# Kernel tuning notes

Hardware: AMD Instinct MI355X
Metric: run time of the kernel (lower is better)

The kernel has to match this reference:

```python
import jax, jax.numpy as jnp
import numpy as np

T, D, H, O = 16384, 512, 1024, 512


def setup_inputs() -> dict:
    key = jax.random.key(0)
    k_in, k_h0, kU, kW, kV = jax.random.split(key, 5)
    inputs = jax.random.randint(k_in, (T,), 0, D)
    h0 = jax.random.normal(k_h0, (H,), dtype=jnp.float32)
    U = jax.random.normal(kU, (H, D), dtype=jnp.float32) * 0.01
    W = jax.random.normal(kW, (H, H), dtype=jnp.float32) * 0.01
    V = jax.random.normal(kV, (O, H), dtype=jnp.float32) * 0.01
    bh = jnp.zeros((H,), dtype=jnp.float32)
    by = jnp.zeros((O,), dtype=jnp.float32)
    return {"inputs": inputs, "h0": h0, "U": U, "W": W, "V": V, "bh": bh, "by": by}


def reference(inputs, h0, U, W, V, bh, by):
    # U @ one_hot(x_t) is just a column gather of U; precompute for all t: (T, H)
    Ux = U.T[inputs]

    def step(h, ux):
        h = jnp.tanh(ux + W @ h + bh)  # (H,)
        return h, h

    h_T, hs = jax.lax.scan(step, h0, Ux)  # hs: (T, H)
    logits = hs @ V.T + by  # (T, O)
    return logits, h_T
```

## Files before the change

kernel.cpp:

```cpp
#include <hip/hip_runtime.h>
#include <cstdint>


constexpr int T_STEPS = 16384;
constexpr int D_DIM   = 512;
constexpr int H_DIM   = 1024;
constexpr int O_DIM   = 512;
constexpr int NBLK    = 32;
constexpr int NTHR    = 512;

__device__ __forceinline__ float fast_tanh(float x) {
    float e = __expf(2.f * x);
    return 1.f - 2.f / (e + 1.f);
}

__device__ __forceinline__ float hsum4(const float4& v) {
    return (v.x + v.y) + (v.z + v.w);
}

__global__ __launch_bounds__(NTHR, 2)
void rnn_fused(const int* __restrict__ xs, const float* __restrict__ h0,
               const float* __restrict__ U, const float* __restrict__ W,
               const float* __restrict__ V, const float* __restrict__ bh,
               const float* __restrict__ by, float* __restrict__ out,
               unsigned long long* __restrict__ htag)
{
    const int b   = blockIdx.x;
    const int tid = threadIdx.x;
    const int w   = tid >> 6;
    const int l   = tid & 63;

    __shared__ float hl[2][H_DIM];

    const int wr0 = b * 32 + w * 4;
    float4 wreg[4][4];
#pragma unroll
    for (int j = 0; j < 4; ++j)
#pragma unroll
        for (int q = 0; q < 4; ++q)
            wreg[j][q] = *(const float4*)(W + (size_t)(wr0 + j) * H_DIM + 16 * l + 4 * q);
    const float bh_r = bh[wr0 + (l & 3)];
    const int   urow = wr0 + (l & 3);

    const int vr0 = b * 16 + w * 2;
    float4 vreg[2][4];
#pragma unroll
    for (int m = 0; m < 2; ++m)
#pragma unroll
        for (int q = 0; q < 4; ++q)
            vreg[m][q] = *(const float4*)(V + (size_t)(vr0 + m) * H_DIM + 16 * l + 4 * q);
    const float by_r = by[vr0 + (l & 1)];

    int rdw[4];
#pragma unroll
    for (int q = 0; q < 4; ++q)
        rdw[q] = 16 * l + 4 * (q ^ ((l >> 1) & 3));
    const int c   = tid >> 3;
    const int qw  = (tid >> 1) & 3;
    const int wdw = 16 * c + 4 * (qw ^ ((c >> 1) & 3)) + 2 * (tid & 1);

    const bool o1 = (l & 1) != 0, o2 = (l & 2) != 0;

    for (int t = 0; t < T_STEPS; ++t) {
        const int sb = (~t) & 1;
        float* hb = hl[sb];

        const int   xt = xs[t];
        const float uv = U[(size_t)urow * D_DIM + xt];

        float2 hpair;
        if (t == 0) {
            hpair = *(const float2*)(h0 + 2 * tid);
        } else {
            const unsigned want = (unsigned)(t - 1);
            const unsigned long long* pp = htag + (size_t)((t - 1) & 1) * H_DIM + 2 * tid;
            unsigned long long q0, q1;
            do {
                q0 = __hip_atomic_load(pp + 0, __ATOMIC_RELAXED, __HIP_MEMORY_SCOPE_AGENT);
                q1 = __hip_atomic_load(pp + 1, __ATOMIC_RELAXED, __HIP_MEMORY_SCOPE_AGENT);
            } while ((unsigned)(q0 >> 32) != want || (unsigned)(q1 >> 32) != want);
            hpair = make_float2(__uint_as_float((unsigned)q0),
                                __uint_as_float((unsigned)q1));
        }
        *(float2*)&hb[wdw] = hpair;
        __syncthreads();

        float4 h4[4];
#pragma unroll
        for (int q = 0; q < 4; ++q) h4[q] = *(const float4*)&hb[rdw[q]];

        float s[4];
#pragma unroll
        for (int j = 0; j < 4; ++j) {
            float4 a = make_float4(0.f, 0.f, 0.f, 0.f);
#pragma unroll
            for (int q = 0; q < 4; ++q) {
                a.x += wreg[j][q].x * h4[q].x;
                a.y += wreg[j][q].y * h4[q].y;
                a.z += wreg[j][q].z * h4[q].z;
                a.w += wreg[j][q].w * h4[q].w;
            }
            s[j] = hsum4(a);
        }
        float A  = o1 ? s[1] : s[0], Ax = o1 ? s[0] : s[1];
        float B  = o1 ? s[3] : s[2], Bx = o1 ? s[2] : s[3];
        A += __shfl_xor(Ax, 1);
        B += __shfl_xor(Bx, 1);
        float Cv = o2 ? B : A, Cx = o2 ? A : B;
        Cv += __shfl_xor(Cx, 2);
        Cv += __shfl_xor(Cv, 4);
        Cv += __shfl_xor(Cv, 8);
        Cv += __shfl_xor(Cv, 16);
        Cv += __shfl_xor(Cv, 32);

        const float hv = fast_tanh(Cv + bh_r + uv);
        if (l < 4) {
            const unsigned long long pk =
                ((unsigned long long)(unsigned)t << 32) | (unsigned long long)__float_as_uint(hv);
            __hip_atomic_store(htag + (size_t)(t & 1) * H_DIM + wr0 + l, pk,
                               __ATOMIC_RELAXED, __HIP_MEMORY_SCOPE_AGENT);
        }

        if (t > 0) {
            float sv[2];
#pragma unroll
            for (int m = 0; m < 2; ++m) {
                float4 a = make_float4(0.f, 0.f, 0.f, 0.f);
#pragma unroll
                for (int q = 0; q < 4; ++q) {
                    a.x += vreg[m][q].x * h4[q].x;
                    a.y += vreg[m][q].y * h4[q].y;
                    a.z += vreg[m][q].z * h4[q].z;
                    a.w += vreg[m][q].w * h4[q].w;
                }
                sv[m] = hsum4(a);
            }
            float P  = o1 ? sv[1] : sv[0], Px = o1 ? sv[0] : sv[1];
            P += __shfl_xor(Px, 1);
            P += __shfl_xor(P, 2);
            P += __shfl_xor(P, 4);
            P += __shfl_xor(P, 8);
            P += __shfl_xor(P, 16);
            P += __shfl_xor(P, 32);
            if (l < 2) out[(size_t)(t - 1) * O_DIM + vr0 + l] = P + by_r;
        }
    }

    {
        const unsigned want = (unsigned)(T_STEPS - 1);
        const unsigned long long* pp = htag + (size_t)((T_STEPS - 1) & 1) * H_DIM + 2 * tid;
        unsigned long long q0, q1;
        do {
            q0 = __hip_atomic_load(pp + 0, __ATOMIC_RELAXED, __HIP_MEMORY_SCOPE_AGENT);
            q1 = __hip_atomic_load(pp + 1, __ATOMIC_RELAXED, __HIP_MEMORY_SCOPE_AGENT);
        } while ((unsigned)(q0 >> 32) != want || (unsigned)(q1 >> 32) != want);
        float2 hpair = make_float2(__uint_as_float((unsigned)q0),
                                   __uint_as_float((unsigned)q1));
        if (b == 0)
            *(float2*)&out[(size_t)T_STEPS * O_DIM + 2 * tid] = hpair;

        float* hb = hl[1];
        *(float2*)&hb[wdw] = hpair;
        __syncthreads();
        float4 h4[4];
#pragma unroll
        for (int q = 0; q < 4; ++q) h4[q] = *(const float4*)&hb[rdw[q]];
        float sv[2];
#pragma unroll
        for (int m = 0; m < 2; ++m) {
            float4 a = make_float4(0.f, 0.f, 0.f, 0.f);
#pragma unroll
            for (int q = 0; q < 4; ++q) {
                a.x += vreg[m][q].x * h4[q].x;
                a.y += vreg[m][q].y * h4[q].y;
                a.z += vreg[m][q].z * h4[q].z;
                a.w += vreg[m][q].w * h4[q].w;
            }
            sv[m] = hsum4(a);
        }
        float P  = o1 ? sv[1] : sv[0], Px = o1 ? sv[0] : sv[1];
        P += __shfl_xor(Px, 1);
        P += __shfl_xor(P, 2);
        P += __shfl_xor(P, 4);
        P += __shfl_xor(P, 8);
        P += __shfl_xor(P, 16);
        P += __shfl_xor(P, 32);
        if (l < 2) out[(size_t)(T_STEPS - 1) * O_DIM + vr0 + l] = P + by_r;
    }
}

extern "C" void kernel_launch(void* const* d_in, const int* in_sizes, int n_in,
                              void* d_out, int out_size, void* d_ws, size_t ws_size,
                              hipStream_t stream) {
    const int*   xs = (const int*)d_in[0];
    const float* h0 = (const float*)d_in[1];
    const float* U  = (const float*)d_in[2];
    const float* W  = (const float*)d_in[3];
    const float* V  = (const float*)d_in[4];
    const float* bh = (const float*)d_in[5];
    const float* by = (const float*)d_in[6];
    float* out = (float*)d_out;

    unsigned long long* htag = (unsigned long long*)d_ws;
    hipMemsetAsync(d_ws, 0xAA, 2 * H_DIM * sizeof(unsigned long long), stream);

    rnn_fused<<<NBLK, NTHR, 0, stream>>>(xs, h0, U, W, V, bh, by, out, htag);
}
```

Measured before the change: 23.19 ms.

## Have each wave poll the full hidden vector directly, dropping LDS staging and barrier

Each wavefront now loads the entire tagged hidden state from global memory with inline-asm system-coherent dwordx4 loads, checked wave-wide with __all. This replaces the per-thread partial poll followed by an LDS exchange and __syncthreads. It removes the block-wide barrier and the LDS round trip from the serial critical path of every timestep. In exchange each wave issues 8x more polling traffic against the shared workspace, and the weight layout is reorganized into float2 slices.

```diff
diff --git a/kernel.cpp b/kernel.cpp
--- a/kernel.cpp
+++ b/kernel.cpp
@@ -9,16 +9,18 @@
 constexpr int NBLK    = 32;
 constexpr int NTHR    = 512;
 
+typedef unsigned int u32x4 __attribute__((ext_vector_type(4)));
+
 __device__ __forceinline__ float fast_tanh(float x) {
     float e = __expf(2.f * x);
     return 1.f - 2.f / (e + 1.f);
 }
 
-__device__ __forceinline__ float hsum4(const float4& v) {
-    return (v.x + v.y) + (v.z + v.w);
-}
-
-__global__ __launch_bounds__(NTHR, 2)
+#define POLL_ISSUE(reg, addr)                                          \
+    asm volatile("global_load_dwordx4 %0, %1, off sc0 sc1"             \
+                 : "=v"(reg) : "v"((unsigned long long)(addr)))
+
+__global__ __launch_bounds__(NTHR, 1)
 void rnn_fused(const int* __restrict__ xs, const float* __restrict__ h0,
                const float* __restrict__ U, const float* __restrict__ W,
                const float* __restrict__ V, const float* __restrict__ bh,
@@ -30,80 +32,74 @@
     const int w   = tid >> 6;
     const int l   = tid & 63;
 
-    __shared__ float hl[2][H_DIM];
-
     const int wr0 = b * 32 + w * 4;
-    float4 wreg[4][4];
+    float2 wreg[4][8];
 #pragma unroll
     for (int j = 0; j < 4; ++j)
 #pragma unroll
-        for (int q = 0; q < 4; ++q)
-            wreg[j][q] = *(const float4*)(W + (size_t)(wr0 + j) * H_DIM + 16 * l + 4 * q);
+        for (int i = 0; i < 8; ++i)
+            wreg[j][i] = *(const float2*)(W + (size_t)(wr0 + j) * H_DIM + 128 * i + 2 * l);
     const float bh_r = bh[wr0 + (l & 3)];
     const int   urow = wr0 + (l & 3);
 
     const int vr0 = b * 16 + w * 2;
-    float4 vreg[2][4];
+    float2 vreg[2][8];
 #pragma unroll
     for (int m = 0; m < 2; ++m)
 #pragma unroll
-        for (int q = 0; q < 4; ++q)
-            vreg[m][q] = *(const float4*)(V + (size_t)(vr0 + m) * H_DIM + 16 * l + 4 * q);
+        for (int i = 0; i < 8; ++i)
+            vreg[m][i] = *(const float2*)(V + (size_t)(vr0 + m) * H_DIM + 128 * i + 2 * l);
     const float by_r = by[vr0 + (l & 1)];
 
-    int rdw[4];
-#pragma unroll
-    for (int q = 0; q < 4; ++q)
-        rdw[q] = 16 * l + 4 * (q ^ ((l >> 1) & 3));
-    const int c   = tid >> 3;
-    const int qw  = (tid >> 1) & 3;
-    const int wdw = 16 * c + 4 * (qw ^ ((c >> 1) & 3)) + 2 * (tid & 1);
+    const unsigned long long* gp0 = htag + 2 * l;
+    const unsigned long long* gp1 = htag + H_DIM + 2 * l;
 
     const bool o1 = (l & 1) != 0, o2 = (l & 2) != 0;
 
+    float2 h2[8];
+
     for (int t = 0; t < T_STEPS; ++t) {
-        const int sb = (~t) & 1;
-        float* hb = hl[sb];
-
         const int   xt = xs[t];
         const float uv = U[(size_t)urow * D_DIM + xt];
 
-        float2 hpair;
         if (t == 0) {
-            hpair = *(const float2*)(h0 + 2 * tid);
+#pragma unroll
+            for (int i = 0; i < 8; ++i)
+                h2[i] = *(const float2*)(h0 + 128 * i + 2 * l);
         } else {
+            const unsigned long long* pp = ((t - 1) & 1) ? gp1 : gp0;
             const unsigned want = (unsigned)(t - 1);
-            const unsigned long long* pp = htag + (size_t)((t - 1) & 1) * H_DIM + 2 * tid;
-            unsigned long long q0, q1;
-            do {
-                q0 = __hip_atomic_load(pp + 0, __ATOMIC_RELAXED, __HIP_MEMORY_SCOPE_AGENT);
-                q1 = __hip_atomic_load(pp + 1, __ATOMIC_RELAXED, __HIP_MEMORY_SCOPE_AGENT);
-            } while ((unsigned)(q0 >> 32) != want || (unsigned)(q1 >> 32) != want);
-            hpair = make_float2(__uint_as_float((unsigned)q0),
-                                __uint_as_float((unsigned)q1));
-        }
-        *(float2*)&hb[wdw] = hpair;
-        __syncthreads();
-
-        float4 h4[4];
-#pragma unroll
-        for (int q = 0; q < 4; ++q) h4[q] = *(const float4*)&hb[rdw[q]];
-
-        float s[4];
-#pragma unroll
-        for (int j = 0; j < 4; ++j) {
-            float4 a = make_float4(0.f, 0.f, 0.f, 0.f);
-#pragma unroll
-            for (int q = 0; q < 4; ++q) {
-                a.x += wreg[j][q].x * h4[q].x;
-                a.y += wreg[j][q].y * h4[q].y;
-                a.z += wreg[j][q].z * h4[q].z;
-                a.w += wreg[j][q].w * h4[q].w;
+            u32x4 q[8];
+            for (;;) {
+#pragma unroll
+                for (int i = 0; i < 8; ++i) POLL_ISSUE(q[i], pp + 128 * i);
+                asm volatile("s_waitcnt vmcnt(0)" ::: "memory");
+                __builtin_amdgcn_sched_barrier(0);
+                bool ok = true;
+#pragma unroll
+                for (int i = 0; i < 8; ++i)
+                    ok = ok && (q[i].y == want) && (q[i].w == want);
+                if (__all(ok)) break;
             }
-            s[j] = hsum4(a);
-        }
-        float A  = o1 ? s[1] : s[0], Ax = o1 ? s[0] : s[1];
-        float B  = o1 ? s[3] : s[2], Bx = o1 ? s[2] : s[3];
+#pragma unroll
+            for (int i = 0; i < 8; ++i)
+                h2[i] = make_float2(__uint_as_float(q[i].x),
+                                    __uint_as_float(q[i].z));
+        }
+
+        float2 a0 = {0.f, 0.f}, a1 = {0.f, 0.f}, a2 = {0.f, 0.f}, a3 = {0.f, 0.f};
+#pragma unroll
+        for (int i = 0; i < 8; ++i) {
+            a0.x += wreg[0][i].x * h2[i].x; a0.y += wreg[0][i].y * h2[i].y;
+            a1.x += wreg[1][i].x * h2[i].x; a1.y += wreg[1][i].y * h2[i].y;
+            a2.x += wreg[2][i].x * h2[i].x; a2.y += wreg[2][i].y * h2[i].y;
+            a3.x += wreg[3][i].x * h2[i].x; a3.y += wreg[3][i].y * h2[i].y;
+        }
+        const float s0 = a0.x + a0.y, s1 = a1.x + a1.y;
+        const float s2 = a2.x + a2.y, s3 = a3.x + a3.y;
+
+        float A  = o1 ? s1 : s0, Ax = o1 ? s0 : s1;
+        float B  = o1 ? s3 : s2, Bx = o1 ? s2 : s3;
         A += __shfl_xor(Ax, 1);
         B += __shfl_xor(Bx, 1);
         float Cv = o2 ? B : A, Cx = o2 ? A : B;
@@ -116,26 +112,22 @@
         const float hv = fast_tanh(Cv + bh_r + uv);
         if (l < 4) {
             const unsigned long long pk =
-                ((unsigned long long)(unsigned)t << 32) | (unsigned long long)__float_as_uint(hv);
+                ((unsigned long long)(unsigned)t << 32) |
+                (unsigned long long)__float_as_uint(hv);
             __hip_atomic_store(htag + (size_t)(t & 1) * H_DIM + wr0 + l, pk,
                                __ATOMIC_RELAXED, __HIP_MEMORY_SCOPE_AGENT);
         }
+        __builtin_amdgcn_sched_barrier(0);
 
         if (t > 0) {
-            float sv[2];
-#pragma unroll
-            for (int m = 0; m < 2; ++m) {
-                float4 a = make_float4(0.f, 0.f, 0.f, 0.f);
-#pragma unroll
-                for (int q = 0; q < 4; ++q) {
-                    a.x += vreg[m][q].x * h4[q].x;
-                    a.y += vreg[m][q].y * h4[q].y;
-                    a.z += vreg[m][q].z * h4[q].z;
-                    a.w += vreg[m][q].w * h4[q].w;
-                }
-                sv[m] = hsum4(a);
+            float2 p0 = {0.f, 0.f}, p1 = {0.f, 0.f};
+#pragma unroll
+            for (int i = 0; i < 8; ++i) {
+                p0.x += vreg[0][i].x * h2[i].x; p0.y += vreg[0][i].y * h2[i].y;
+                p1.x += vreg[1][i].x * h2[i].x; p1.y += vreg[1][i].y * h2[i].y;
             }
-            float P  = o1 ? sv[1] : sv[0], Px = o1 ? sv[0] : sv[1];
+            const float sv0 = p0.x + p0.y, sv1 = p1.x + p1.y;
+            float P  = o1 ? sv1 : sv0, Px = o1 ? sv0 : sv1;
             P += __shfl_xor(Px, 1);
             P += __shfl_xor(P, 2);
             P += __shfl_xor(P, 4);
@@ -147,38 +139,39 @@
     }
 
     {
+        const unsigned long long* pp = gp1;
         const unsigned want = (unsigned)(T_STEPS - 1);
-        const unsigned long long* pp = htag + (size_t)((T_STEPS - 1) & 1) * H_DIM + 2 * tid;
-        unsigned long long q0, q1;
-        do {
-            q0 = __hip_atomic_load(pp + 0, __ATOMIC_RELAXED, __HIP_MEMORY_SCOPE_AGENT);
-            q1 = __hip_atomic_load(pp + 1, __ATOMIC_RELAXED, __HIP_MEMORY_SCOPE_AGENT);
-        } while ((unsigned)(q0 >> 32) != want || (unsigned)(q1 >> 32) != want);
-        float2 hpair = make_float2(__uint_as_float((unsigned)q0),
-                                   __uint_as_float((unsigned)q1));
-        if (b == 0)
-            *(float2*)&out[(size_t)T_STEPS * O_DIM + 2 * tid] = hpair;
-
-        float* hb = hl[1];
-        *(float2*)&hb[wdw] = hpair;
-        __syncthreads();
-        float4 h4[4];
-#pragma unroll
-        for (int q = 0; q < 4; ++q) h4[q] = *(const float4*)&hb[rdw[q]];
-        float sv[2];
-#pragma unroll
-        for (int m = 0; m < 2; ++m) {
-            float4 a = make_float4(0.f, 0.f, 0.f, 0.f);
-#pragma unroll
-            for (int q = 0; q < 4; ++q) {
-                a.x += vreg[m][q].x * h4[q].x;
-                a.y += vreg[m][q].y * h4[q].y;
-                a.z += vreg[m][q].z * h4[q].z;
-                a.w += vreg[m][q].w * h4[q].w;
-            }
-            sv[m] = hsum4(a);
-        }
-        float P  = o1 ? sv[1] : sv[0], Px = o1 ? sv[0] : sv[1];
+        u32x4 q[8];
+        for (;;) {
+#pragma unroll
+            for (int i = 0; i < 8; ++i) POLL_ISSUE(q[i], pp + 128 * i);
+            asm volatile("s_waitcnt vmcnt(0)" ::: "memory");
+            __builtin_amdgcn_sched_barrier(0);
+            bool ok = true;
+#pragma unroll
+            for (int i = 0; i < 8; ++i)
+                ok = ok && (q[i].y == want) && (q[i].w == want);
+            if (__all(ok)) break;
+        }
+#pragma unroll
+        for (int i = 0; i < 8; ++i)
+            h2[i] = make_float2(__uint_as_float(q[i].x),
+                                __uint_as_float(q[i].z));
+
+        if (b == 0 && w == 0) {
+#pragma unroll
+            for (int i = 0; i < 8; ++i)
+                *(float2*)&out[(size_t)T_STEPS * O_DIM + 128 * i + 2 * l] = h2[i];
+        }
+
+        float2 p0 = {0.f, 0.f}, p1 = {0.f, 0.f};
+#pragma unroll
+        for (int i = 0; i < 8; ++i) {
+            p0.x += vreg[0][i].x * h2[i].x; p0.y += vreg[0][i].y * h2[i].y;
+            p1.x += vreg[1][i].x * h2[i].x; p1.y += vreg[1][i].y * h2[i].y;
+        }
+        const float sv0 = p0.x + p0.y, sv1 = p1.x + p1.y;
+        float P  = o1 ? sv1 : sv0, Px = o1 ? sv0 : sv1;
         P += __shfl_xor(Px, 1);
         P += __shfl_xor(P, 2);
         P += __shfl_xor(P, 4);
```

New measurement: 40.19 ms. 1.73x slower.
